# Kernel tuning notes

Hardware: AMD Instinct MI355X
Metric: run time of the kernel (lower is better)

The kernel has to match this reference:

```python
import jax, jax.numpy as jnp
import numpy as np

N_NODES = 100000
N_EDGES = 1600000
IN_CH = 256
HID_CH = 32
OUT_CH = 8
N_GRAPHS = 64


def gcn_conv(x, edge_index, W, b):
    # PyG GCNConv: linear transform, add self-loops, symmetric norm, scatter-add.
    xw = x @ W  # [N, C_out]
    src, dst = edge_index[0], edge_index[1]
    loop = jnp.arange(N_NODES, dtype=src.dtype)
    src_f = jnp.concatenate([src, loop])  # [E+N]
    dst_f = jnp.concatenate([dst, loop])
    # degree over targets including self-loops (edge weight 1)
    deg = jax.ops.segment_sum(jnp.ones_like(dst_f, dtype=xw.dtype), dst_f,
                              num_segments=N_NODES)
    dinv = jnp.where(deg > 0, jax.lax.rsqrt(deg), 0.0)
    norm = dinv[src_f] * dinv[dst_f]  # [E+N]
    msgs = xw[src_f] * norm[:, None]  # gather + scale
    out = jax.ops.segment_sum(msgs, dst_f, num_segments=N_NODES)
    return out + b


def setup_inputs() -> dict:
    key = jax.random.key(0)
    k1, k2, k3, k4, k5, k6 = jax.random.split(key, 6)
    x = jax.random.normal(k1, (N_NODES, IN_CH), dtype=jnp.float32)
    edge_index = jax.random.randint(k2, (2, N_EDGES), 0, N_NODES, dtype=jnp.int64)
    batch = jnp.sort(jax.random.randint(k3, (N_NODES,), 0, N_GRAPHS, dtype=jnp.int64))
    s1 = 1.0 / np.sqrt(IN_CH)
    s2 = 1.0 / np.sqrt(HID_CH)
    W1 = jax.random.uniform(k4, (IN_CH, HID_CH), jnp.float32, -s1, s1)
    b1 = jnp.zeros((HID_CH,), jnp.float32)
    W2 = jax.random.uniform(k5, (HID_CH, OUT_CH), jnp.float32, -s2, s2)
    b2 = jnp.zeros((OUT_CH,), jnp.float32)
    return {"x": x, "edge_index": edge_index, "batch": batch,
            "W1": W1, "b1": b1, "W2": W2, "b2": b2}


def reference(x, edge_index, batch, W1, b1, W2, b2):
    h = jax.nn.relu(gcn_conv(x, edge_index, W1, b1))   # [N, HID]
    h = jax.nn.relu(gcn_conv(h, edge_index, W2, b2))   # [N, OUT]
    # global mean pool per graph
    sums = jax.ops.segment_sum(h, batch, num_segments=N_GRAPHS)
    cnts = jax.ops.segment_sum(jnp.ones((h.shape[0],), h.dtype), batch,
                               num_segments=N_GRAPHS)
    pooled = sums / jnp.maximum(cnts, 1.0)[:, None]    # [G, OUT]
    return jax.nn.log_softmax(pooled, axis=1)
```

## Files before the change

### kernel.cpp

```cpp
#include <hip/hip_runtime.h>
#include <hip/hip_bf16.h>
#include <math.h>

#define N_NODES 100000
#define N_EDGES 1600000
#define IN_CH 256
#define HID_CH 32
#define OUT_CH 8
#define N_GRAPHS 64

#define BUCK_SHIFT 7
#define NODES_PER_BUCK 128
#define NBUCK ((N_NODES + NODES_PER_BUCK - 1) / NODES_PER_BUCK)
#define CAP 2560
#define PCAP 3456
#define CHUNK 2048
#define NBLK_P1 ((N_EDGES + CHUNK - 1) / CHUNK)
#define ARENA (NBUCK * CAP)

#define DUMMY_ROW N_NODES
#define Y_ROWS 100008

#define GM_NODES 64
#define XPITCH 264

#define OFF_DEG    0
#define OFF_DINV   (OFF_DEG + N_NODES)
#define OFF_ROWS   (OFF_DINV + N_NODES)
#define OFF_CNTG   (OFF_ROWS + N_NODES)
#define OFF_CSR    (OFF_CNTG + 784)
#define OFF_Y1     (OFF_CSR + NBUCK*PCAP)
#define OFF_BBUF   (OFF_Y1 + Y_ROWS*16)
#define OFF_Y2     (OFF_BBUF + ARENA)
#define OFF_PSUM   (OFF_Y2 + Y_ROWS*4)
#define OFF_PCNT   (OFF_PSUM + N_GRAPHS*OUT_CH)

typedef __attribute__((ext_vector_type(8))) short bf16x8;
typedef __attribute__((ext_vector_type(4))) float f32x4;

__device__ __forceinline__ unsigned bfr(float f) {
    unsigned u = __float_as_uint(f);
    return (u + 0x7fffu + ((u >> 16) & 1u)) >> 16;
}
__device__ __forceinline__ float bf_lo(unsigned w) { return __uint_as_float(w << 16); }
__device__ __forceinline__ float bf_hi(unsigned w) { return __uint_as_float(w & 0xffff0000u); }

#define ACC8(r) do { \
    a0 += bf_lo((r).x); a1 += bf_hi((r).x); a2 += bf_lo((r).y); a3 += bf_hi((r).y); \
    a4 += bf_lo((r).z); a5 += bf_hi((r).z); a6 += bf_lo((r).w); a7 += bf_hi((r).w); } while (0)

__global__ void zero_kernel(unsigned* __restrict__ cntg, unsigned* __restrict__ y1w,
                            unsigned* __restrict__ y2w) {
    const int t = threadIdx.x;
    for (int i = t; i < NBUCK; i += 256) cntg[i] = 0u;
    if (t < 16) y1w[(size_t)DUMMY_ROW * 16 + t] = 0u;
    if (t < 4)  y2w[(size_t)DUMMY_ROW * 4 + t] = 0u;
}

__global__ __launch_bounds__(256) void p1_partition(
        const int* __restrict__ src, const int* __restrict__ dst,
        unsigned* __restrict__ cntg, unsigned* __restrict__ bbuf) {
    __shared__ unsigned hcnt[NBUCK];
    __shared__ unsigned hcur[NBUCK];
    const int t = threadIdx.x;
    const long long e0 = (long long)blockIdx.x * CHUNK;

    int rs[8]; unsigned rd[8];
#pragma unroll
    for (int i = 0; i < 8; i++) {
        const long long e = e0 + t + i * 256;
        const bool v = (e < N_EDGES);
        rs[i] = v ? src[e] : 0;
        rd[i] = v ? (unsigned)dst[e] : 0xFFFFFFFFu;
    }
    for (int i = t; i < NBUCK; i += 256) hcnt[i] = 0;
    __syncthreads();
#pragma unroll
    for (int i = 0; i < 8; i++)
        if (rd[i] != 0xFFFFFFFFu) atomicAdd(&hcnt[rd[i] >> BUCK_SHIFT], 1u);
    __syncthreads();
    for (int i = t; i < NBUCK; i += 256) {
        const unsigned c = hcnt[i];
        const unsigned r = c ? atomicAdd(&cntg[i], c) : 0u;
        hcur[i] = (unsigned)i * CAP + r;
    }
    __syncthreads();
#pragma unroll
    for (int i = 0; i < 8; i++) {
        if (rd[i] != 0xFFFFFFFFu) {
            const unsigned b = rd[i] >> BUCK_SHIFT;
            const unsigned pos = atomicAdd(&hcur[b], 1u);
            if (pos - b * CAP < CAP)
                bbuf[pos] = (unsigned)rs[i] | ((rd[i] & (NODES_PER_BUCK - 1)) << 17);
        }
    }
}

__global__ __launch_bounds__(256) void p2_build(
        const unsigned* __restrict__ cntg,
        const unsigned* __restrict__ bbuf, int* __restrict__ csr,
        unsigned* __restrict__ deg, unsigned* __restrict__ rowstart,
        float* __restrict__ dinv) {
    __shared__ unsigned hist[NODES_PER_BUCK];
    __shared__ unsigned start[NODES_PER_BUCK];
    __shared__ unsigned cur[NODES_PER_BUCK];
    __shared__ unsigned s[256];
    __shared__ int lcsr[PCAP];
    const int b = blockIdx.x;
    const int t = threadIdx.x;
    unsigned cnt = cntg[b]; if (cnt > CAP) cnt = CAP;
    const unsigned* mybuf = bbuf + (size_t)b * CAP;

    if (t < NODES_PER_BUCK) hist[t] = 0;
    __syncthreads();
    for (unsigned i = t; i < cnt; i += 256) atomicAdd(&hist[mybuf[i] >> 17], 1u);
    __syncthreads();
    const unsigned d = (t < NODES_PER_BUCK) ? hist[t] : 0u;
    const unsigned pd = (d + 7u) & ~7u;
    s[t] = pd;
    __syncthreads();
    for (int off = 1; off < 256; off <<= 1) {
        unsigned x = (t >= off) ? s[t - off] : 0u;
        __syncthreads();
        s[t] += x;
        __syncthreads();
    }
    const unsigned total = s[255];
    const unsigned ex = s[t] - pd;
    if (t < NODES_PER_BUCK) { start[t] = ex; cur[t] = ex; }
    __syncthreads();
    for (unsigned i = t; i < total; i += 256) lcsr[i] = DUMMY_ROW;
    __syncthreads();
    for (unsigned i = t; i < cnt; i += 256) {
        const unsigned p = mybuf[i];
        const unsigned pos = atomicAdd(&cur[p >> 17], 1u);
        lcsr[pos] = (int)(p & 0x1FFFFu);
    }
    __syncthreads();
    const unsigned gbase = (unsigned)b * PCAP;
    for (unsigned i = t; i < total; i += 256) csr[gbase + i] = lcsr[i];
    const int n = b * NODES_PER_BUCK + t;
    if (t < NODES_PER_BUCK && n < N_NODES) {
        deg[n] = d;
        rowstart[n] = gbase + start[t];
        dinv[n] = rsqrtf((float)d + 1.0f);
    }
}

__global__ __launch_bounds__(256) void gemm1_kernel(
        const float* __restrict__ x, const float* __restrict__ W1,
        const float* __restrict__ dinv, unsigned short* __restrict__ y1bf,
        float* __restrict__ psum) {
    __shared__ unsigned short xs[GM_NODES * XPITCH];
    const int t = threadIdx.x;

    if (blockIdx.x == 0) {
        for (int i = t; i < N_GRAPHS * OUT_CH + N_GRAPHS; i += 256) psum[i] = 0.0f;
    }

    const int node0 = blockIdx.x * GM_NODES;
    const int w = t >> 6;
    const int lane = t & 63;
    const int lr = lane & 15;
    const int lg = lane >> 4;

    bf16x8 bw[8][2];
#pragma unroll
    for (int kb = 0; kb < 8; kb++) {
#pragma unroll
        for (int cb = 0; cb < 2; cb++) {
#pragma unroll
            for (int j = 0; j < 8; j++)
                bw[kb][cb][j] = (short)bfr(W1[(kb * 32 + lg * 8 + j) * 32 + cb * 16 + lr]);
        }
    }

    const float4* xv = (const float4*)x;
#pragma unroll
    for (int i = 0; i < 8; i++) {
        const int idx = t + i * 256;
        const int row = idx >> 5, k8 = idx & 31;
        int gr = node0 + row; if (gr >= N_NODES) gr = N_NODES - 1;
        const float4 A = xv[(size_t)gr * 64 + k8 * 2];
        const float4 B = xv[(size_t)gr * 64 + k8 * 2 + 1];
        uint4 pk;
        pk.x = bfr(A.x) | (bfr(A.y) << 16);
        pk.y = bfr(A.z) | (bfr(A.w) << 16);
        pk.z = bfr(B.x) | (bfr(B.y) << 16);
        pk.w = bfr(B.z) | (bfr(B.w) << 16);
        *(uint4*)((char*)xs + row * 528 + k8 * 16) = pk;
    }
    __syncthreads();

    f32x4 acc0 = {0.f, 0.f, 0.f, 0.f}, acc1 = {0.f, 0.f, 0.f, 0.f};
#pragma unroll
    for (int kb = 0; kb < 8; kb++) {
        const bf16x8 a = *(const bf16x8*)((const char*)xs + (w * 16 + lr) * 528 + kb * 64 + lg * 16);
        acc0 = __builtin_amdgcn_mfma_f32_16x16x32_bf16(a, bw[kb][0], acc0, 0, 0, 0);
        acc1 = __builtin_amdgcn_mfma_f32_16x16x32_bf16(a, bw[kb][1], acc1, 0, 0, 0);
    }

#pragma unroll
    for (int r = 0; r < 4; r++) {
        const int n = node0 + w * 16 + lg * 4 + r;
        if (n < N_NODES) {
            const float dv = dinv[n];
            y1bf[(size_t)n * 32 + lr]      = (unsigned short)bfr(acc0[r] * dv);
            y1bf[(size_t)n * 32 + 16 + lr] = (unsigned short)bfr(acc1[r] * dv);
        }
    }
}

__global__ __launch_bounds__(256) void g32l2_kernel(
        const unsigned* __restrict__ rowstart, const unsigned* __restrict__ deg,
        const int* __restrict__ csr, const uint4* __restrict__ y1v4,
        const float* __restrict__ dinv, const float* __restrict__ b1,
        const float* __restrict__ W2, uint4* __restrict__ y2v4) {
    __shared__ float w2s[HID_CH][9];
    __shared__ float b1s[HID_CH];
    const int t = threadIdx.x;
    { const int k = t >> 3, c = t & 7; w2s[k][c] = W2[t]; }
    if (t < HID_CH) b1s[t] = b1[t];
    __syncthreads();

    const int nl = t >> 2;
    const int q = t & 3;
    const int node = blockIdx.x * 64 + nl;
    if (node >= N_NODES) return;
    const int b4 = (t & 63) & ~3;

    const unsigned d = deg[node];
    const unsigned pd = (d + 7u) & ~7u;
    const unsigned base = rowstart[node];

    float a0, a1, a2, a3, a4, a5, a6, a7;
    { const uint4 sv = y1v4[(size_t)node * 4 + q];
      a0 = bf_lo(sv.x); a1 = bf_hi(sv.x); a2 = bf_lo(sv.y); a3 = bf_hi(sv.y);
      a4 = bf_lo(sv.z); a5 = bf_hi(sv.z); a6 = bf_lo(sv.w); a7 = bf_hi(sv.w); }

    unsigned j = 0;
    for (; j + 16 <= pd; j += 16) {
        const int4 e4 = ((const int4*)(csr + base + j))[q];
        const int s0  = __shfl(e4.x, b4 + 0);
        const int s1  = __shfl(e4.y, b4 + 0);
        const int s2  = __shfl(e4.z, b4 + 0);
        const int s3  = __shfl(e4.w, b4 + 0);
        const int s4  = __shfl(e4.x, b4 + 1);
        const int s5  = __shfl(e4.y, b4 + 1);
        const int s6  = __shfl(e4.z, b4 + 1);
        const int s7  = __shfl(e4.w, b4 + 1);
        const int s8  = __shfl(e4.x, b4 + 2);
        const int s9  = __shfl(e4.y, b4 + 2);
        const int s10 = __shfl(e4.z, b4 + 2);
        const int s11 = __shfl(e4.w, b4 + 2);
        const int s12 = __shfl(e4.x, b4 + 3);
        const int s13 = __shfl(e4.y, b4 + 3);
        const int s14 = __shfl(e4.z, b4 + 3);
        const int s15 = __shfl(e4.w, b4 + 3);
        const uint4 r0  = y1v4[(size_t)s0 * 4 + q];
        const uint4 r1  = y1v4[(size_t)s1 * 4 + q];
        const uint4 r2  = y1v4[(size_t)s2 * 4 + q];
        const uint4 r3  = y1v4[(size_t)s3 * 4 + q];
        const uint4 r4  = y1v4[(size_t)s4 * 4 + q];
        const uint4 r5  = y1v4[(size_t)s5 * 4 + q];
        const uint4 r6  = y1v4[(size_t)s6 * 4 + q];
        const uint4 r7  = y1v4[(size_t)s7 * 4 + q];
        const uint4 r8  = y1v4[(size_t)s8 * 4 + q];
        const uint4 r9  = y1v4[(size_t)s9 * 4 + q];
        const uint4 r10 = y1v4[(size_t)s10 * 4 + q];
        const uint4 r11 = y1v4[(size_t)s11 * 4 + q];
        const uint4 r12 = y1v4[(size_t)s12 * 4 + q];
        const uint4 r13 = y1v4[(size_t)s13 * 4 + q];
        const uint4 r14 = y1v4[(size_t)s14 * 4 + q];
        const uint4 r15 = y1v4[(size_t)s15 * 4 + q];
        ACC8(r0);  ACC8(r1);  ACC8(r2);  ACC8(r3);
        ACC8(r4);  ACC8(r5);  ACC8(r6);  ACC8(r7);
        ACC8(r8);  ACC8(r9);  ACC8(r10); ACC8(r11);
        ACC8(r12); ACC8(r13); ACC8(r14); ACC8(r15);
    }
    if (j < pd) {
        const int4 e4 = ((const int4*)(csr + base + j))[q & 1];
        const int s0 = __shfl(e4.x, b4);
        const int s1 = __shfl(e4.y, b4);
        const int s2 = __shfl(e4.z, b4);
        const int s3 = __shfl(e4.w, b4);
        const int s4 = __shfl(e4.x, b4 + 1);
        const int s5 = __shfl(e4.y, b4 + 1);
        const int s6 = __shfl(e4.z, b4 + 1);
        const int s7 = __shfl(e4.w, b4 + 1);
        const uint4 r0 = y1v4[(size_t)s0 * 4 + q];
        const uint4 r1 = y1v4[(size_t)s1 * 4 + q];
        const uint4 r2 = y1v4[(size_t)s2 * 4 + q];
        const uint4 r3 = y1v4[(size_t)s3 * 4 + q];
        const uint4 r4 = y1v4[(size_t)s4 * 4 + q];
        const uint4 r5 = y1v4[(size_t)s5 * 4 + q];
        const uint4 r6 = y1v4[(size_t)s6 * 4 + q];
        const uint4 r7 = y1v4[(size_t)s7 * 4 + q];
        ACC8(r0); ACC8(r1); ACC8(r2); ACC8(r3);
        ACC8(r4); ACC8(r5); ACC8(r6); ACC8(r7);
    }

    const float dv = dinv[node];
    float h[8];
    h[0] = fmaxf(fmaf(a0, dv, b1s[8 * q + 0]), 0.0f);
    h[1] = fmaxf(fmaf(a1, dv, b1s[8 * q + 1]), 0.0f);
    h[2] = fmaxf(fmaf(a2, dv, b1s[8 * q + 2]), 0.0f);
    h[3] = fmaxf(fmaf(a3, dv, b1s[8 * q + 3]), 0.0f);
    h[4] = fmaxf(fmaf(a4, dv, b1s[8 * q + 4]), 0.0f);
    h[5] = fmaxf(fmaf(a5, dv, b1s[8 * q + 5]), 0.0f);
    h[6] = fmaxf(fmaf(a6, dv, b1s[8 * q + 6]), 0.0f);
    h[7] = fmaxf(fmaf(a7, dv, b1s[8 * q + 7]), 0.0f);

    float p[8] = {0, 0, 0, 0, 0, 0, 0, 0};
#pragma unroll
    for (int i = 0; i < 8; i++) {
        const float hi = h[i];
#pragma unroll
        for (int c = 0; c < 8; c++) p[c] = fmaf(hi, w2s[8 * q + i][c], p[c]);
    }
#pragma unroll
    for (int c = 0; c < 8; c++) p[c] += __shfl_xor(p[c], 1);
#pragma unroll
    for (int c = 0; c < 8; c++) p[c] += __shfl_xor(p[c], 2);

    if (q == 0) {
        uint4 pk;
        pk.x = bfr(p[0] * dv) | (bfr(p[1] * dv) << 16);
        pk.y = bfr(p[2] * dv) | (bfr(p[3] * dv) << 16);
        pk.z = bfr(p[4] * dv) | (bfr(p[5] * dv) << 16);
        pk.w = bfr(p[6] * dv) | (bfr(p[7] * dv) << 16);
        y2v4[node] = pk;
    }
}

__global__ __launch_bounds__(256) void g8pool_kernel(
        const unsigned* __restrict__ rowstart, const unsigned* __restrict__ deg,
        const int* __restrict__ csr, const uint4* __restrict__ y2v4,
        const float* __restrict__ dinv, const float* __restrict__ b2,
        const int* __restrict__ batch,
        float* __restrict__ psum, float* __restrict__ pcnt) {
    __shared__ float ls[N_GRAPHS * OUT_CH];
    __shared__ float lc[N_GRAPHS];
    __shared__ float b2s[OUT_CH];
    __shared__ int grange[2];
    __shared__ float tr[32][8][9];
    const int t = threadIdx.x;
    ls[t] = 0.0f; ls[t + 256] = 0.0f;
    if (t < N_GRAPHS) lc[t] = 0.0f;
    if (t < OUT_CH) b2s[t] = b2[t];
    if (t == 0) { grange[0] = N_GRAPHS; grange[1] = -1; }
    __syncthreads();

    const int nl = t >> 3;
    const int l = t & 7;
    const int node = blockIdx.x * 32 + nl;
    const int g = batch[node];
    const unsigned d = deg[node];
    const unsigned pd = (d + 7u) & ~7u;
    const unsigned base = rowstart[node];

    float a0 = 0, a1 = 0, a2 = 0, a3 = 0, a4 = 0, a5 = 0, a6 = 0, a7 = 0;
    if (l == 0) { const uint4 sv = y2v4[node]; ACC8(sv); }
    for (unsigned j = 0; j < pd; j += 8) {
        const int si = csr[base + j + l];
        const uint4 r = y2v4[si];
        ACC8(r);
    }
    tr[nl][l][0] = a0; tr[nl][l][1] = a1; tr[nl][l][2] = a2; tr[nl][l][3] = a3;
    tr[nl][l][4] = a4; tr[nl][l][5] = a5; tr[nl][l][6] = a6; tr[nl][l][7] = a7;
    __syncthreads();
    float sc = 0.0f;
#pragma unroll
    for (int i = 0; i < 8; i++) sc += tr[nl][i][l];

    const float o = fmaxf(fmaf(sc, dinv[node], b2s[l]), 0.0f);
    atomicAdd(&ls[g * OUT_CH + l], o);
    if (l == 0) {
        atomicAdd(&lc[g], 1.0f);
        atomicMin(&grange[0], g);
        atomicMax(&grange[1], g);
    }
    __syncthreads();
    const int g0 = grange[0], g1 = grange[1];
    const int nent = (g1 - g0 + 1) * OUT_CH;
    for (int i = t; i < nent; i += 256)
        atomicAdd(&psum[g0 * OUT_CH + i], ls[g0 * OUT_CH + i]);
    for (int i = t; i < g1 - g0 + 1; i += 256)
        atomicAdd(&pcnt[g0 + i], lc[g0 + i]);
}

__global__ void logsoftmax_kernel(const float* __restrict__ psum,
                                  const float* __restrict__ pcnt,
                                  float* __restrict__ out) {
    const int g = threadIdx.x;
    if (g >= N_GRAPHS) return;
    const float cnt = fmaxf(pcnt[g], 1.0f);
    float p[OUT_CH];
    float m = -INFINITY;
#pragma unroll
    for (int c = 0; c < OUT_CH; c++) {
        p[c] = psum[g * OUT_CH + c] / cnt;
        m = fmaxf(m, p[c]);
    }
    float s = 0.0f;
#pragma unroll
    for (int c = 0; c < OUT_CH; c++) s += expf(p[c] - m);
    const float lse = logf(s);
#pragma unroll
    for (int c = 0; c < OUT_CH; c++) out[g * OUT_CH + c] = p[c] - m - lse;
}

extern "C" void kernel_launch(void* const* d_in, const int* in_sizes, int n_in,
                              void* d_out, int out_size, void* d_ws, size_t ws_size,
                              hipStream_t stream) {
    const float* x    = (const float*)d_in[0];
    const int* eidx   = (const int*)d_in[1];
    const int* batch  = (const int*)d_in[2];
    const float* W1   = (const float*)d_in[3];
    const float* b1   = (const float*)d_in[4];
    const float* W2   = (const float*)d_in[5];
    const float* b2   = (const float*)d_in[6];
    float* out = (float*)d_out;

    const int* src = eidx;
    const int* dst = eidx + N_EDGES;

    char* wsb = (char*)d_ws;
    unsigned* deg   = (unsigned*)(wsb) + OFF_DEG;
    float*    dinv  = (float*)(wsb) + OFF_DINV;
    unsigned* rows  = (unsigned*)(wsb) + OFF_ROWS;
    unsigned* cntg  = (unsigned*)(wsb) + OFF_CNTG;
    int*      csr   = (int*)(wsb) + OFF_CSR;
    unsigned* y1w   = (unsigned*)(wsb) + OFF_Y1;
    unsigned* bbuf  = (unsigned*)(wsb) + OFF_BBUF;
    unsigned* y2w   = (unsigned*)(wsb) + OFF_Y2;
    float*    psum  = (float*)(wsb) + OFF_PSUM;
    float*    pcnt  = (float*)(wsb) + OFF_PCNT;

    zero_kernel<<<1, 256, 0, stream>>>(cntg, y1w, y2w);
    p1_partition<<<NBLK_P1, 256, 0, stream>>>(src, dst, cntg, bbuf);
    p2_build<<<NBUCK, 256, 0, stream>>>(cntg, bbuf, csr, deg, rows, dinv);
    gemm1_kernel<<<(N_NODES + GM_NODES - 1) / GM_NODES, 256, 0, stream>>>(
        x, W1, dinv, (unsigned short*)y1w, psum);
    g32l2_kernel<<<(N_NODES + 63) / 64, 256, 0, stream>>>(rows, deg, csr, (const uint4*)y1w,
                                                          dinv, b1, W2, (uint4*)y2w);
    g8pool_kernel<<<N_NODES / 32, 256, 0, stream>>>(rows, deg, csr, (const uint4*)y2w,
                                                    dinv, b2, batch, psum, pcnt);
    logsoftmax_kernel<<<1, 64, 0, stream>>>(psum, pcnt, out);
}
```

Before: 128.8 us.

## Precompute W1 MFMA fragments once and load x directly into MFMA operands

A new prep kernel converts W1 to bf16 MFMA fragment layout once, replacing the zero kernel. The gemm1 kernel then loads ready-made fragments instead of having every block gather and convert W1 from fp32. The gemm1 kernel also drops its LDS staging of x: each wave handles its own 16-node tile and reads x rows straight into registers. This removes the shared-memory round trip and barrier, but the global loads become less coalesced, since each lane reads 32-byte pieces spread across rows.

Result: no change. 128.5 us (-0.2%).

```diff
diff --git a/kernel.cpp b/kernel.cpp
--- a/kernel.cpp
+++ b/kernel.cpp
@@ -20,9 +20,6 @@
 
 #define DUMMY_ROW N_NODES
 #define Y_ROWS 100008
-
-#define GM_NODES 64
-#define XPITCH 264
 
 #define OFF_DEG    0
 #define OFF_DINV   (OFF_DEG + N_NODES)
@@ -34,6 +31,7 @@
 #define OFF_Y2     (OFF_BBUF + ARENA)
 #define OFF_PSUM   (OFF_Y2 + Y_ROWS*4)
 #define OFF_PCNT   (OFF_PSUM + N_GRAPHS*OUT_CH)
+#define OFF_WFRAG  (OFF_PCNT + 128)
 
 typedef __attribute__((ext_vector_type(8))) short bf16x8;
 typedef __attribute__((ext_vector_type(4))) float f32x4;
@@ -49,12 +47,30 @@
     a0 += bf_lo((r).x); a1 += bf_hi((r).x); a2 += bf_lo((r).y); a3 += bf_hi((r).y); \
     a4 += bf_lo((r).z); a5 += bf_hi((r).z); a6 += bf_lo((r).w); a7 += bf_hi((r).w); } while (0)
 
-__global__ void zero_kernel(unsigned* __restrict__ cntg, unsigned* __restrict__ y1w,
-                            unsigned* __restrict__ y2w) {
-    const int t = threadIdx.x;
-    for (int i = t; i < NBUCK; i += 256) cntg[i] = 0u;
-    if (t < 16) y1w[(size_t)DUMMY_ROW * 16 + t] = 0u;
-    if (t < 4)  y2w[(size_t)DUMMY_ROW * 4 + t] = 0u;
+__global__ __launch_bounds__(256) void wprep_kernel(
+        const float* __restrict__ W1, uint4* __restrict__ wfrag,
+        unsigned* __restrict__ cntg, unsigned* __restrict__ y1w,
+        unsigned* __restrict__ y2w) {
+    const int t = threadIdx.x;
+    if (blockIdx.x == 0) {
+        for (int i = t; i < NBUCK; i += 256) cntg[i] = 0u;
+        if (t < 16) y1w[(size_t)DUMMY_ROW * 16 + t] = 0u;
+        if (t < 4)  y2w[(size_t)DUMMY_ROW * 4 + t] = 0u;
+    }
+    const int fl = blockIdx.x * 256 + t;
+    const int f = fl >> 6, lane = fl & 63;
+    const int kb = f >> 1, cb = f & 1;
+    const int lr = lane & 15, lg = lane >> 4;
+    unsigned short s[8];
+#pragma unroll
+    for (int j = 0; j < 8; j++)
+        s[j] = (unsigned short)bfr(W1[(kb * 32 + lg * 8 + j) * 32 + cb * 16 + lr]);
+    uint4 pk;
+    pk.x = s[0] | ((unsigned)s[1] << 16);
+    pk.y = s[2] | ((unsigned)s[3] << 16);
+    pk.z = s[4] | ((unsigned)s[5] << 16);
+    pk.w = s[6] | ((unsigned)s[7] << 16);
+    wfrag[fl] = pk;
 }
 
 __global__ __launch_bounds__(256) void p1_partition(
@@ -148,19 +164,18 @@
 }
 
 __global__ __launch_bounds__(256) void gemm1_kernel(
-        const float* __restrict__ x, const float* __restrict__ W1,
+        const float* __restrict__ x, const uint4* __restrict__ wfrag,
         const float* __restrict__ dinv, unsigned short* __restrict__ y1bf,
         float* __restrict__ psum) {
-    __shared__ unsigned short xs[GM_NODES * XPITCH];
-    const int t = threadIdx.x;
-
+    const int t = threadIdx.x;
     if (blockIdx.x == 0) {
         for (int i = t; i < N_GRAPHS * OUT_CH + N_GRAPHS; i += 256) psum[i] = 0.0f;
     }
-
-    const int node0 = blockIdx.x * GM_NODES;
     const int w = t >> 6;
     const int lane = t & 63;
+    const int tile = blockIdx.x * 4 + w;
+    if (tile >= N_NODES / 16) return;
+    const int node0 = tile * 16;
     const int lr = lane & 15;
     const int lg = lane >> 4;
 
@@ -169,45 +184,32 @@
     for (int kb = 0; kb < 8; kb++) {
 #pragma unroll
         for (int cb = 0; cb < 2; cb++) {
-#pragma unroll
-            for (int j = 0; j < 8; j++)
-                bw[kb][cb][j] = (short)bfr(W1[(kb * 32 + lg * 8 + j) * 32 + cb * 16 + lr]);
+            const uint4 v = wfrag[(kb * 2 + cb) * 64 + lane];
+            bw[kb][cb] = *(const bf16x8*)&v;
         }
     }
 
-    const float4* xv = (const float4*)x;
-#pragma unroll
-    for (int i = 0; i < 8; i++) {
-        const int idx = t + i * 256;
-        const int row = idx >> 5, k8 = idx & 31;
-        int gr = node0 + row; if (gr >= N_NODES) gr = N_NODES - 1;
-        const float4 A = xv[(size_t)gr * 64 + k8 * 2];
-        const float4 B = xv[(size_t)gr * 64 + k8 * 2 + 1];
-        uint4 pk;
-        pk.x = bfr(A.x) | (bfr(A.y) << 16);
-        pk.y = bfr(A.z) | (bfr(A.w) << 16);
-        pk.z = bfr(B.x) | (bfr(B.y) << 16);
-        pk.w = bfr(B.z) | (bfr(B.w) << 16);
-        *(uint4*)((char*)xs + row * 528 + k8 * 16) = pk;
-    }
-    __syncthreads();
-
+    const float4* xr = (const float4*)(x + (size_t)(node0 + lr) * IN_CH);
     f32x4 acc0 = {0.f, 0.f, 0.f, 0.f}, acc1 = {0.f, 0.f, 0.f, 0.f};
 #pragma unroll
     for (int kb = 0; kb < 8; kb++) {
-        const bf16x8 a = *(const bf16x8*)((const char*)xs + (w * 16 + lr) * 528 + kb * 64 + lg * 16);
+        const float4 A = xr[kb * 8 + lg * 2];
+        const float4 B = xr[kb * 8 + lg * 2 + 1];
+        bf16x8 a;
+        a[0] = (short)bfr(A.x); a[1] = (short)bfr(A.y);
+        a[2] = (short)bfr(A.z); a[3] = (short)bfr(A.w);
+        a[4] = (short)bfr(B.x); a[5] = (short)bfr(B.y);
+        a[6] = (short)bfr(B.z); a[7] = (short)bfr(B.w);
         acc0 = __builtin_amdgcn_mfma_f32_16x16x32_bf16(a, bw[kb][0], acc0, 0, 0, 0);
         acc1 = __builtin_amdgcn_mfma_f32_16x16x32_bf16(a, bw[kb][1], acc1, 0, 0, 0);
     }
 
 #pragma unroll
     for (int r = 0; r < 4; r++) {
-        const int n = node0 + w * 16 + lg * 4 + r;
-        if (n < N_NODES) {
-            const float dv = dinv[n];
-            y1bf[(size_t)n * 32 + lr]      = (unsigned short)bfr(acc0[r] * dv);
-            y1bf[(size_t)n * 32 + 16 + lr] = (unsigned short)bfr(acc1[r] * dv);
-        }
+        const int n = node0 + lg * 4 + r;
+        const float dv = dinv[n];
+        y1bf[(size_t)n * 32 + lr]      = (unsigned short)bfr(acc0[r] * dv);
+        y1bf[(size_t)n * 32 + 16 + lr] = (unsigned short)bfr(acc1[r] * dv);
     }
 }
 
@@ -436,12 +438,13 @@
     unsigned* y2w   = (unsigned*)(wsb) + OFF_Y2;
     float*    psum  = (float*)(wsb) + OFF_PSUM;
     float*    pcnt  = (float*)(wsb) + OFF_PCNT;
-
-    zero_kernel<<<1, 256, 0, stream>>>(cntg, y1w, y2w);
+    uint4*    wfrag = (uint4*)((unsigned*)(wsb) + OFF_WFRAG);
+
+    wprep_kernel<<<4, 256, 0, stream>>>(W1, wfrag, cntg, y1w, y2w);
     p1_partition<<<NBLK_P1, 256, 0, stream>>>(src, dst, cntg, bbuf);
     p2_build<<<NBUCK, 256, 0, stream>>>(cntg, bbuf, csr, deg, rows, dinv);
-    gemm1_kernel<<<(N_NODES + GM_NODES - 1) / GM_NODES, 256, 0, stream>>>(
-        x, W1, dinv, (unsigned short*)y1w, psum);
+    gemm1_kernel<<<(N_NODES / 16 + 3) / 4, 256, 0, stream>>>(
+        x, wfrag, dinv, (unsigned short*)y1w, psum);
     g32l2_kernel<<<(N_NODES + 63) / 64, 256, 0, stream>>>(rows, deg, csr, (const uint4*)y1w,
                                                           dinv, b1, W2, (uint4*)y2w);
     g8pool_kernel<<<N_NODES / 32, 256, 0, stream>>>(rows, deg, csr, (const uint4*)y2w,
```
